# Kernel optimization log

Hardware: AMD Instinct MI355X
Metric: run time of the kernel (lower is better)

## Reference

```python
import jax, jax.numpy as jnp
import numpy as np

PATCH = 3
COMPLETENESS = 2.0


def setup_inputs() -> dict:
    key = jax.random.key(0)
    k1, k2, k3 = jax.random.split(key, 3)
    C, Hs, Ws, Hr, Wr = 64, 512, 512, 512, 512
    ref = jax.random.normal(k1, (C, Hr, Wr), dtype=jnp.float32)
    nnf_sr = jax.random.randint(k2, (Hs, Ws, 2), 0, 512, dtype=jnp.int32)  # (ry, rx) per src pixel
    nnf_rs = jax.random.randint(k3, (Hr, Wr, 2), 0, 512, dtype=jnp.int32)  # (sy, sx) per ref pixel
    return {"ref": ref, "nnf_sr": nnf_sr, "nnf_rs": nnf_rs}


def bds_vote(ref, nnf_sr, nnf_rs, patch=PATCH, completeness=COMPLETENESS):
    C, Hr, Wr = ref.shape
    Hs, Ws = nnf_sr.shape[0], nnf_sr.shape[1]
    h = patch // 2
    ws = 1.0 / (Hs * Ws)
    wr = completeness / (Hr * Wr)

    guide = jnp.zeros((C, Hs * Ws), dtype=ref.dtype)
    weight = jnp.zeros((Hs * Ws,), dtype=ref.dtype)

    def accumulate(guide, weight, sy, sx, ry, rx, w):
        # sy,sx: target (src) centers [N]; ry,rx: source (ref) centers [N]
        # Clipped patch extents of the original code are equivalent to per-pixel
        # validity: both target and ref offset coords must be in range.
        for dy in range(-h, h + 1):
            for dx in range(-h, h + 1):
                ty, tx = sy + dy, sx + dx
                qy, qx = ry + dy, rx + dx
                valid = ((ty >= 0) & (ty < Hs) & (tx >= 0) & (tx < Ws) &
                         (qy >= 0) & (qy < Hr) & (qx >= 0) & (qx < Wr))
                vmask = valid.astype(ref.dtype) * w
                idx = jnp.clip(ty, 0, Hs - 1) * Ws + jnp.clip(tx, 0, Ws - 1)
                vals = ref[:, jnp.clip(qy, 0, Hr - 1), jnp.clip(qx, 0, Wr - 1)] * vmask[None, :]
                guide = guide.at[:, idx].add(vals)
                weight = weight.at[idx].add(vmask)
        return guide, weight

    # source -> reference pass (weight ws)
    gy, gx = jnp.meshgrid(jnp.arange(Hs), jnp.arange(Ws), indexing='ij')
    guide, weight = accumulate(guide, weight,
                               gy.reshape(-1), gx.reshape(-1),
                               nnf_sr[..., 0].reshape(-1), nnf_sr[..., 1].reshape(-1), ws)
    # reference -> source pass (weight wr)
    ry, rx = jnp.meshgrid(jnp.arange(Hr), jnp.arange(Wr), indexing='ij')
    guide, weight = accumulate(guide, weight,
                               nnf_rs[..., 0].reshape(-1), nnf_rs[..., 1].reshape(-1),
                               ry.reshape(-1), rx.reshape(-1), wr)

    weight = jnp.where(weight == 0, jnp.asarray(1.0, ref.dtype), weight)
    return (guide / weight[None, :]).reshape(C, Hs, Ws)


def reference(ref, nnf_sr, nnf_rs):
    return bds_vote(ref, nnf_sr, nnf_rs)
```

## Files before the change

### kernel.cpp

```cpp
#include <hip/hip_runtime.h>

#define HS   512
#define WSZ  512
#define NC   64
#define HW   (HS * WSZ)
#define KCAP 16
#define LCAP 32

typedef unsigned int uint;
typedef unsigned short ushort;

__device__ __forceinline__ ushort f2bf(float f) {
    uint b = __float_as_uint(f);
    return (ushort)((b + 0x7FFFu + ((b >> 16) & 1u)) >> 16);
}

__global__ __launch_bounds__(256) void prep_kernel(
    const float4* __restrict__ ref4, uint4* __restrict__ refu4,
    int* __restrict__ cnt)
{
    __shared__ float lds[64 * 65];
    const int p0  = blockIdx.x * 64;
    const int tid = threadIdx.x;
    if (tid < 64) cnt[blockIdx.x * 64 + tid] = 0;
#pragma unroll
    for (int k = 0; k < 4; ++k) {
        int e  = k * 256 + tid;
        int c  = e >> 4;
        int i4 = e & 15;
        float4 v = ref4[(size_t)c * (HW / 4) + (p0 >> 2) + i4];
        lds[(i4 * 4 + 0) * 65 + c] = v.x;
        lds[(i4 * 4 + 1) * 65 + c] = v.y;
        lds[(i4 * 4 + 2) * 65 + c] = v.z;
        lds[(i4 * 4 + 3) * 65 + c] = v.w;
    }
    __syncthreads();
#pragma unroll
    for (int k = 0; k < 2; ++k) {
        int e = k * 256 + tid;
        int i = e >> 3;
        int q = e & 7;
        const float* row = &lds[i * 65 + 8 * q];
        uint4 u;
        u.x = (uint)f2bf(row[0]) | ((uint)f2bf(row[1]) << 16);
        u.y = (uint)f2bf(row[2]) | ((uint)f2bf(row[3]) << 16);
        u.z = (uint)f2bf(row[4]) | ((uint)f2bf(row[5]) << 16);
        u.w = (uint)f2bf(row[6]) | ((uint)f2bf(row[7]) << 16);
        refu4[(size_t)(p0 + i) * 8 + q] = u;
    }
}

__global__ __launch_bounds__(256) void fill_bins(
    const int2* __restrict__ nnf_rs, int* __restrict__ cnt,
    int* __restrict__ slots)
{
    int r = blockIdx.x * 256 + threadIdx.x;
    int2 s = nnf_rs[r];
    int bin = (s.x << 9) | s.y;
    int pos = atomicAdd(&cnt[bin], 1);
    if (pos < KCAP) slots[(bin << 4) + pos] = r;
}

__global__ __launch_bounds__(256) void gather_lds(
    const uint4* __restrict__ refu4,
    const int2*  __restrict__ nnf_sr,
    const int*   __restrict__ cnt,
    const int*   __restrict__ slots,
    float* __restrict__ out)
{
    const float ws = 1.0f / 262144.0f;
    const float wr = 2.0f / 262144.0f;

    __shared__ int lists[32][36];
    __shared__ int lcnt[32];
    __shared__ int bcnt[102];

    const int tid = threadIdx.x;
    const int t0  = blockIdx.x * 32;
    const int ty0 = t0 >> 9, tx0 = t0 & 511;

    if (tid < 32) lcnt[tid] = 0;
    if (tid < 102) {
        const int jr = tid / 34, jc = tid - jr * 34;
        const int sy = ty0 + jr - 1, sx = tx0 + jc - 1;
        const bool sv = ((unsigned)sy < 512u) & ((unsigned)sx < 512u);
        bcnt[tid] = sv ? min(cnt[(sy << 9) | sx], KCAP) : 0;
    }
    __syncthreads();

    for (int p = tid; p < 306; p += 256) {
        const int j  = p / 3;
        const int di = p - j * 3;
        const int jr = j / 34, jc = j - jr * 34;
        const int dy = 1 - jr;
        const int dx = di - 1;
        const int lt = jc - 1 + dx;
        const int c  = bcnt[j];
        if (((unsigned)lt < 32u) && (c > 0)) {
            const int sy = ty0 + jr - 1, sx = tx0 + jc - 1;
            const int sbase = (((sy << 9) | sx) << 4);
            for (int e = 0; e < c; ++e) {
                const int r  = slots[sbase + e];
                const int qy = (r >> 9) + dy, qx = (r & 511) + dx;
                if (((unsigned)qy < 512u) & ((unsigned)qx < 512u)) {
                    const int pos = atomicAdd(&lcnt[lt], 1);
                    if (pos < LCAP) lists[lt][pos] = (qy << 9) | qx;
                }
            }
        }
    }
    __syncthreads();

    const int k  = tid & 7;
    const int lt = tid >> 3;
    const int t  = t0 + lt;
    const int ty = ty0, tx = t & 511;

    float a0=0,a1=0,a2=0,a3=0,a4=0,a5=0,a6=0,a7=0, w=0.f;

#define ACCUM(qv, mv)                                                         \
    {                                                                         \
        const int   q_ = (qv);                                                \
        const float m_ = (mv);                                                \
        uint4 u_ = refu4[(size_t)q_ * 8 + k];                                 \
        a0 += __uint_as_float(u_.x << 16)         * m_;                       \
        a1 += __uint_as_float(u_.x & 0xffff0000u) * m_;                       \
        a2 += __uint_as_float(u_.y << 16)         * m_;                       \
        a3 += __uint_as_float(u_.y & 0xffff0000u) * m_;                       \
        a4 += __uint_as_float(u_.z << 16)         * m_;                       \
        a5 += __uint_as_float(u_.z & 0xffff0000u) * m_;                       \
        a6 += __uint_as_float(u_.w << 16)         * m_;                       \
        a7 += __uint_as_float(u_.w & 0xffff0000u) * m_;                       \
        w += m_;                                                              \
    }

#define TAP(dy, dx)                                                           \
    {                                                                         \
        const int sy = ty - (dy), sx = tx - (dx);                             \
        const bool sval = ((unsigned)sy < 512u) & ((unsigned)sx < 512u);      \
        const int sidx = ((sy & 511) << 9) | (sx & 511);                      \
        const int2 nn = nnf_sr[sidx];                                         \
        const int qy = nn.x + (dy), qx = nn.y + (dx);                         \
        const bool v = sval & ((unsigned)qy < 512u) & ((unsigned)qx < 512u);  \
        ACCUM((((qy & 511) << 9) | (qx & 511)), v ? ws : 0.f)                 \
    }

    TAP(-1, -1)  TAP(-1, 0)  TAP(-1, 1)
    TAP( 0, -1)  TAP( 0, 0)  TAP( 0, 1)
    TAP( 1, -1)  TAP( 1, 0)  TAP( 1, 1)
#undef TAP

    const int S = min(lcnt[lt], LCAP);
    for (int s = 0; s < S; s += 4) {
        const int4 e4 = *(const int4*)&lists[lt][s];
        ACCUM(e4.x & 0x3FFFF, wr)
        ACCUM(e4.y & 0x3FFFF, (s + 1 < S) ? wr : 0.f)
        ACCUM(e4.z & 0x3FFFF, (s + 2 < S) ? wr : 0.f)
        ACCUM(e4.w & 0x3FFFF, (s + 3 < S) ? wr : 0.f)
    }
#undef ACCUM

    if (w == 0.f) w = 1.f;
    const float inv = 1.f / w;
    size_t o = (size_t)(8 * k) * HW + t;
    out[o]                = a0 * inv;
    out[o + 1*(size_t)HW] = a1 * inv;
    out[o + 2*(size_t)HW] = a2 * inv;
    out[o + 3*(size_t)HW] = a3 * inv;
    out[o + 4*(size_t)HW] = a4 * inv;
    out[o + 5*(size_t)HW] = a5 * inv;
    out[o + 6*(size_t)HW] = a6 * inv;
    out[o + 7*(size_t)HW] = a7 * inv;
}

__global__ __launch_bounds__(256) void gather8_f32(
    const float* __restrict__ reff,
    const int2*  __restrict__ nnf_sr,
    const int*   __restrict__ cnt,
    const int*   __restrict__ slots,
    float* __restrict__ out)
{
    const float ws = 1.0f / 262144.0f;
    const float wr = 2.0f / 262144.0f;

    const int tid = threadIdx.x;
    const int k   = tid & 7;
    const int t   = blockIdx.x * 32 + (tid >> 3);
    const int ty  = t >> 9, tx = t & 511;

    float a0=0,a1=0,a2=0,a3=0,a4=0,a5=0,a6=0,a7=0, w=0.f;

#define ACCUM(qv, mv)                                                         \
    {                                                                         \
        const int   q_ = (qv);                                                \
        const float m_ = (mv);                                                \
        const size_t c0_ = (size_t)(8 * k) * HW + q_;                         \
        a0 += reff[c0_ + 0*(size_t)HW] * m_;                                  \
        a1 += reff[c0_ + 1*(size_t)HW] * m_;                                  \
        a2 += reff[c0_ + 2*(size_t)HW] * m_;                                  \
        a3 += reff[c0_ + 3*(size_t)HW] * m_;                                  \
        a4 += reff[c0_ + 4*(size_t)HW] * m_;                                  \
        a5 += reff[c0_ + 5*(size_t)HW] * m_;                                  \
        a6 += reff[c0_ + 6*(size_t)HW] * m_;                                  \
        a7 += reff[c0_ + 7*(size_t)HW] * m_;                                  \
        w += m_;                                                              \
    }

    int mt0,mt1,mt2,mt3,mt4,mt5,mt6,mt7,mt8;
    int run = 0;

#define TAP(i, dy, dx)                                                        \
    {                                                                         \
        const int sy = ty - (dy), sx = tx - (dx);                             \
        const bool sval = ((unsigned)sy < 512u) & ((unsigned)sx < 512u);      \
        const int sidx = ((sy & 511) << 9) | (sx & 511);                      \
        mt##i = (sidx << 12) | ((i) << 8) | run;                              \
        const int c = cnt[sidx];                                              \
        run += sval ? min(c, KCAP) : 0;                                       \
        const int2 nn = nnf_sr[sidx];                                         \
        const int qy = nn.x + (dy), qx = nn.y + (dx);                         \
        const bool v = sval & ((unsigned)qy < 512u) & ((unsigned)qx < 512u);  \
        ACCUM((((qy & 511) << 9) | (qx & 511)), v ? ws : 0.f)                 \
    }

    TAP(0, -1, -1)  TAP(1, -1, 0)  TAP(2, -1, 1)
    TAP(3,  0, -1)  TAP(4,  0, 0)  TAP(5,  0, 1)
    TAP(6,  1, -1)  TAP(7,  1, 0)  TAP(8,  1, 1)
#undef TAP

    const int S = run;

#define SEL(i)  m_ = (s_ >= (mt##i & 255)) ? mt##i : m_;
#define ENTRY(sv)                                                             \
    {                                                                         \
        const int s_ = (sv);                                                  \
        int m_ = mt0;                                                         \
        SEL(1) SEL(2) SEL(3) SEL(4) SEL(5) SEL(6) SEL(7) SEL(8)               \
        const int off_ = m_ & 255;                                            \
        const int ii_  = (m_ >> 8) & 15;                                      \
        const int bs_  = (m_ >> 12) << 4;                                     \
        const int idx_ = min(s_ - off_, KCAP - 1);                            \
        const int e_   = slots[bs_ + idx_];                                   \
        const int ry_  = (e_ >> 9) & 511, rx_ = e_ & 511;                     \
        const int dyp_ = (ii_ * 11) >> 5;                                     \
        const int dy_  = dyp_ - 1, dx_ = ii_ - 3 * dyp_ - 1;                  \
        const int qy_  = ry_ + dy_, qx_ = rx_ + dx_;                          \
        const bool v_  = (s_ < S) &                                           \
                         ((unsigned)qy_ < 512u) & ((unsigned)qx_ < 512u);     \
        ACCUM((((qy_ & 511) << 9) | (qx_ & 511)), v_ ? wr : 0.f)              \
    }

    for (int s = 0; s < S; s += 2) {
        ENTRY(s)
        ENTRY(s + 1)
    }
#undef ENTRY
#undef SEL
#undef ACCUM

    if (w == 0.f) w = 1.f;
    const float inv = 1.f / w;
    size_t o = (size_t)(8 * k) * HW + t;
    out[o]                = a0 * inv;
    out[o + 1*(size_t)HW] = a1 * inv;
    out[o + 2*(size_t)HW] = a2 * inv;
    out[o + 3*(size_t)HW] = a3 * inv;
    out[o + 4*(size_t)HW] = a4 * inv;
    out[o + 5*(size_t)HW] = a5 * inv;
    out[o + 6*(size_t)HW] = a6 * inv;
    out[o + 7*(size_t)HW] = a7 * inv;
}

extern "C" void kernel_launch(void* const* d_in, const int* in_sizes, int n_in,
                              void* d_out, int out_size, void* d_ws, size_t ws_size,
                              hipStream_t stream)
{
    const float* ref    = (const float*)d_in[0];
    const int2*  nnf_sr = (const int2*)d_in[1];
    const int2*  nnf_rs = (const int2*)d_in[2];
    float* out = (float*)d_out;

    char* wsb = (char*)d_ws;
    const size_t refT_bytes = (size_t)HW * NC * 2;
    const size_t cnt_bytes  = (size_t)HW * 4;
    const size_t slot_bytes = (size_t)HW * KCAP * 4;

    if (ws_size >= refT_bytes + cnt_bytes + slot_bytes) {
        uint4* refu4 = (uint4*)wsb;
        int*   cntp  = (int*)(wsb + refT_bytes);
        int*   slots = (int*)(wsb + refT_bytes + cnt_bytes);

        prep_kernel<<<HW / 64, 256, 0, stream>>>((const float4*)ref, refu4, cntp);
        fill_bins<<<HW / 256, 256, 0, stream>>>(nnf_rs, cntp, slots);
        gather_lds<<<HW / 32, 256, 0, stream>>>(refu4, nnf_sr, cntp, slots, out);
    } else {
        int* cntp  = (int*)wsb;
        int* slots = cntp + HW;
        hipMemsetAsync(cntp, 0, cnt_bytes, stream);
        fill_bins<<<HW / 256, 256, 0, stream>>>(nnf_rs, cntp, slots);
        gather8_f32<<<HW / 32, 256, 0, stream>>>(ref, nnf_sr, cntp, slots, out);
    }
}
```

Baseline: 227.4 us.

## Merge prep and bin fill into one launch; sentinel-padded unweighted accumulation

Merges the bf16 transpose kernel and the nnf_rs binning kernel into one launch, with blocks split by index, and zeroes the counts with a memset instead. In the gather kernel, the block's 102 source NNF entries are staged in LDS. Invalid taps and list padding now read a zero sentinel row instead of multiplying by a weight mask, so accumulation becomes plain adds. The ws/wr weights are applied once at the end from valid-entry counts. The costs are one extra memset launch and a workspace row of zeros, and the single final scale may round slightly differently from the per-tap weighting.

Result: faster. 217.5 us (-4.3%).

```diff
diff --git a/kernel.cpp b/kernel.cpp
--- a/kernel.cpp
+++ b/kernel.cpp
@@ -6,6 +6,7 @@
 #define HW   (HS * WSZ)
 #define KCAP 16
 #define LCAP 32
+#define SENT 0x40000
 
 typedef unsigned int uint;
 typedef unsigned short ushort;
@@ -15,50 +16,52 @@
     return (ushort)((b + 0x7FFFu + ((b >> 16) & 1u)) >> 16);
 }
 
-__global__ __launch_bounds__(256) void prep_kernel(
+__global__ __launch_bounds__(256) void prep_fill(
     const float4* __restrict__ ref4, uint4* __restrict__ refu4,
-    int* __restrict__ cnt)
-{
-    __shared__ float lds[64 * 65];
-    const int p0  = blockIdx.x * 64;
-    const int tid = threadIdx.x;
-    if (tid < 64) cnt[blockIdx.x * 64 + tid] = 0;
-#pragma unroll
-    for (int k = 0; k < 4; ++k) {
-        int e  = k * 256 + tid;
-        int c  = e >> 4;
-        int i4 = e & 15;
-        float4 v = ref4[(size_t)c * (HW / 4) + (p0 >> 2) + i4];
-        lds[(i4 * 4 + 0) * 65 + c] = v.x;
-        lds[(i4 * 4 + 1) * 65 + c] = v.y;
-        lds[(i4 * 4 + 2) * 65 + c] = v.z;
-        lds[(i4 * 4 + 3) * 65 + c] = v.w;
-    }
-    __syncthreads();
-#pragma unroll
-    for (int k = 0; k < 2; ++k) {
-        int e = k * 256 + tid;
-        int i = e >> 3;
-        int q = e & 7;
-        const float* row = &lds[i * 65 + 8 * q];
-        uint4 u;
-        u.x = (uint)f2bf(row[0]) | ((uint)f2bf(row[1]) << 16);
-        u.y = (uint)f2bf(row[2]) | ((uint)f2bf(row[3]) << 16);
-        u.z = (uint)f2bf(row[4]) | ((uint)f2bf(row[5]) << 16);
-        u.w = (uint)f2bf(row[6]) | ((uint)f2bf(row[7]) << 16);
-        refu4[(size_t)(p0 + i) * 8 + q] = u;
-    }
-}
-
-__global__ __launch_bounds__(256) void fill_bins(
     const int2* __restrict__ nnf_rs, int* __restrict__ cnt,
     int* __restrict__ slots)
 {
-    int r = blockIdx.x * 256 + threadIdx.x;
-    int2 s = nnf_rs[r];
-    int bin = (s.x << 9) | s.y;
-    int pos = atomicAdd(&cnt[bin], 1);
-    if (pos < KCAP) slots[(bin << 4) + pos] = r;
+    __shared__ float lds[64 * 65];
+    const int tid = threadIdx.x;
+
+    if (blockIdx.x < 4096) {
+        const int p0 = blockIdx.x * 64;
+#pragma unroll
+        for (int k = 0; k < 4; ++k) {
+            int e  = k * 256 + tid;
+            int c  = e >> 4;
+            int i4 = e & 15;
+            float4 v = ref4[(size_t)c * (HW / 4) + (p0 >> 2) + i4];
+            lds[(i4 * 4 + 0) * 65 + c] = v.x;
+            lds[(i4 * 4 + 1) * 65 + c] = v.y;
+            lds[(i4 * 4 + 2) * 65 + c] = v.z;
+            lds[(i4 * 4 + 3) * 65 + c] = v.w;
+        }
+        __syncthreads();
+#pragma unroll
+        for (int k = 0; k < 2; ++k) {
+            int e = k * 256 + tid;
+            int i = e >> 3;
+            int q = e & 7;
+            const float* row = &lds[i * 65 + 8 * q];
+            uint4 u;
+            u.x = (uint)f2bf(row[0]) | ((uint)f2bf(row[1]) << 16);
+            u.y = (uint)f2bf(row[2]) | ((uint)f2bf(row[3]) << 16);
+            u.z = (uint)f2bf(row[4]) | ((uint)f2bf(row[5]) << 16);
+            u.w = (uint)f2bf(row[6]) | ((uint)f2bf(row[7]) << 16);
+            refu4[(size_t)(p0 + i) * 8 + q] = u;
+        }
+    } else {
+        if (blockIdx.x == 4096 && tid < 8) {
+            uint4 z; z.x = 0u; z.y = 0u; z.z = 0u; z.w = 0u;
+            refu4[(size_t)HW * 8 + tid] = z;
+        }
+        const int r = (blockIdx.x - 4096) * 256 + tid;
+        const int2 s = nnf_rs[r];
+        const int bin = (s.x << 9) | s.y;
+        const int pos = atomicAdd(&cnt[bin], 1);
+        if (pos < KCAP) slots[(bin << 4) + pos] = r;
+    }
 }
 
 __global__ __launch_bounds__(256) void gather_lds(
@@ -71,9 +74,10 @@
     const float ws = 1.0f / 262144.0f;
     const float wr = 2.0f / 262144.0f;
 
-    __shared__ int lists[32][36];
-    __shared__ int lcnt[32];
-    __shared__ int bcnt[102];
+    __shared__ __align__(16) int lists[32][36];
+    __shared__ int  lcnt[32];
+    __shared__ int  bcnt[102];
+    __shared__ int2 snn[102];
 
     const int tid = threadIdx.x;
     const int t0  = blockIdx.x * 32;
@@ -84,7 +88,14 @@
         const int jr = tid / 34, jc = tid - jr * 34;
         const int sy = ty0 + jr - 1, sx = tx0 + jc - 1;
         const bool sv = ((unsigned)sy < 512u) & ((unsigned)sx < 512u);
-        bcnt[tid] = sv ? min(cnt[(sy << 9) | sx], KCAP) : 0;
+        const int sidx = ((sy & 511) << 9) | (sx & 511);
+        bcnt[tid] = sv ? min(cnt[sidx], KCAP) : 0;
+        snn[tid]  = nnf_sr[sidx];
+    }
+    {
+        int4 s4; s4.x = SENT; s4.y = SENT; s4.z = SENT; s4.w = SENT;
+        for (int p = tid; p < 288; p += 256)
+            ((int4*)lists)[p] = s4;
     }
     __syncthreads();
 
@@ -113,36 +124,34 @@
 
     const int k  = tid & 7;
     const int lt = tid >> 3;
-    const int t  = t0 + lt;
-    const int ty = ty0, tx = t & 511;
-
-    float a0=0,a1=0,a2=0,a3=0,a4=0,a5=0,a6=0,a7=0, w=0.f;
-
-#define ACCUM(qv, mv)                                                         \
-    {                                                                         \
-        const int   q_ = (qv);                                                \
-        const float m_ = (mv);                                                \
-        uint4 u_ = refu4[(size_t)q_ * 8 + k];                                 \
-        a0 += __uint_as_float(u_.x << 16)         * m_;                       \
-        a1 += __uint_as_float(u_.x & 0xffff0000u) * m_;                       \
-        a2 += __uint_as_float(u_.y << 16)         * m_;                       \
-        a3 += __uint_as_float(u_.y & 0xffff0000u) * m_;                       \
-        a4 += __uint_as_float(u_.z << 16)         * m_;                       \
-        a5 += __uint_as_float(u_.z & 0xffff0000u) * m_;                       \
-        a6 += __uint_as_float(u_.w << 16)         * m_;                       \
-        a7 += __uint_as_float(u_.w & 0xffff0000u) * m_;                       \
-        w += m_;                                                              \
+
+    float a0=0,a1=0,a2=0,a3=0,a4=0,a5=0,a6=0,a7=0;
+    int nv = 0;
+
+#define ACCUM(qv)                                                             \
+    {                                                                         \
+        const uint4 u_ = refu4[(size_t)(qv) * 8 + k];                         \
+        a0 += __uint_as_float(u_.x << 16);                                    \
+        a1 += __uint_as_float(u_.x & 0xffff0000u);                            \
+        a2 += __uint_as_float(u_.y << 16);                                    \
+        a3 += __uint_as_float(u_.y & 0xffff0000u);                            \
+        a4 += __uint_as_float(u_.z << 16);                                    \
+        a5 += __uint_as_float(u_.z & 0xffff0000u);                            \
+        a6 += __uint_as_float(u_.w << 16);                                    \
+        a7 += __uint_as_float(u_.w & 0xffff0000u);                            \
     }
 
 #define TAP(dy, dx)                                                           \
     {                                                                         \
-        const int sy = ty - (dy), sx = tx - (dx);                             \
-        const bool sval = ((unsigned)sy < 512u) & ((unsigned)sx < 512u);      \
-        const int sidx = ((sy & 511) << 9) | (sx & 511);                      \
-        const int2 nn = nnf_sr[sidx];                                         \
+        const bool rv = ((unsigned)(ty0 - (dy)) < 512u);         \
+        const bool cv = ((unsigned)(tx0 + lt - (dx)) < 512u);                 \
+        const int2 nn = snn[(1 - (dy)) * 34 + (lt - (dx) + 1)];               \
         const int qy = nn.x + (dy), qx = nn.y + (dx);                         \
-        const bool v = sval & ((unsigned)qy < 512u) & ((unsigned)qx < 512u);  \
-        ACCUM((((qy & 511) << 9) | (qx & 511)), v ? ws : 0.f)                 \
+        const bool v = rv & cv &                                              \
+                       ((unsigned)qy < 512u) & ((unsigned)qx < 512u);         \
+        const int q = v ? ((qy << 9) | qx) : SENT;                            \
+        nv += v ? 1 : 0;                                                      \
+        ACCUM(q)                                                              \
     }
 
     TAP(-1, -1)  TAP(-1, 0)  TAP(-1, 1)
@@ -150,27 +159,43 @@
     TAP( 1, -1)  TAP( 1, 0)  TAP( 1, 1)
 #undef TAP
 
-    const int S = min(lcnt[lt], LCAP);
-    for (int s = 0; s < S; s += 4) {
+    a0 *= 0.5f; a1 *= 0.5f; a2 *= 0.5f; a3 *= 0.5f;
+    a4 *= 0.5f; a5 *= 0.5f; a6 *= 0.5f; a7 *= 0.5f;
+
+    const int Sreal = min(lcnt[lt], LCAP);
+    const int S4 = (Sreal + 3) & ~3;
+    for (int s = 0; s < S4; s += 4) {
         const int4 e4 = *(const int4*)&lists[lt][s];
-        ACCUM(e4.x & 0x3FFFF, wr)
-        ACCUM(e4.y & 0x3FFFF, (s + 1 < S) ? wr : 0.f)
-        ACCUM(e4.z & 0x3FFFF, (s + 2 < S) ? wr : 0.f)
-        ACCUM(e4.w & 0x3FFFF, (s + 3 < S) ? wr : 0.f)
+        ACCUM(e4.x)
+        ACCUM(e4.y)
+        ACCUM(e4.z)
+        ACCUM(e4.w)
     }
 #undef ACCUM
 
-    if (w == 0.f) w = 1.f;
-    const float inv = 1.f / w;
+    const float wsum = ws * (float)nv + wr * (float)Sreal;
+    const float sc = wr / wsum;
+    const int t = t0 + lt;
     size_t o = (size_t)(8 * k) * HW + t;
-    out[o]                = a0 * inv;
-    out[o + 1*(size_t)HW] = a1 * inv;
-    out[o + 2*(size_t)HW] = a2 * inv;
-    out[o + 3*(size_t)HW] = a3 * inv;
-    out[o + 4*(size_t)HW] = a4 * inv;
-    out[o + 5*(size_t)HW] = a5 * inv;
-    out[o + 6*(size_t)HW] = a6 * inv;
-    out[o + 7*(size_t)HW] = a7 * inv;
+    out[o]                = a0 * sc;
+    out[o + 1*(size_t)HW] = a1 * sc;
+    out[o + 2*(size_t)HW] = a2 * sc;
+    out[o + 3*(size_t)HW] = a3 * sc;
+    out[o + 4*(size_t)HW] = a4 * sc;
+    out[o + 5*(size_t)HW] = a5 * sc;
+    out[o + 6*(size_t)HW] = a6 * sc;
+    out[o + 7*(size_t)HW] = a7 * sc;
+}
+
+__global__ __launch_bounds__(256) void fill_bins(
+    const int2* __restrict__ nnf_rs, int* __restrict__ cnt,
+    int* __restrict__ slots)
+{
+    int r = blockIdx.x * 256 + threadIdx.x;
+    int2 s = nnf_rs[r];
+    int bin = (s.x << 9) | s.y;
+    int pos = atomicAdd(&cnt[bin], 1);
+    if (pos < KCAP) slots[(bin << 4) + pos] = r;
 }
 
 __global__ __launch_bounds__(256) void gather8_f32(
@@ -216,7 +241,7 @@
         const int sidx = ((sy & 511) << 9) | (sx & 511);                      \
         mt##i = (sidx << 12) | ((i) << 8) | run;                              \
         const int c = cnt[sidx];                                              \
-        run += sval ? min(c, KCAP) : 0;                                       \
+        run += sval ? min(c, KCAP) : 0;                                      \
         const int2 nn = nnf_sr[sidx];                                         \
         const int qy = nn.x + (dy), qx = nn.y + (dx);                         \
         const bool v = sval & ((unsigned)qy < 512u) & ((unsigned)qx < 512u);  \
@@ -281,7 +306,7 @@
     float* out = (float*)d_out;
 
     char* wsb = (char*)d_ws;
-    const size_t refT_bytes = (size_t)HW * NC * 2;
+    const size_t refT_bytes = (size_t)HW * NC * 2 + 128;
     const size_t cnt_bytes  = (size_t)HW * 4;
     const size_t slot_bytes = (size_t)HW * KCAP * 4;
 
@@ -290,8 +315,9 @@
         int*   cntp  = (int*)(wsb + refT_bytes);
         int*   slots = (int*)(wsb + refT_bytes + cnt_bytes);
 
-        prep_kernel<<<HW / 64, 256, 0, stream>>>((const float4*)ref, refu4, cntp);
-        fill_bins<<<HW / 256, 256, 0, stream>>>(nnf_rs, cntp, slots);
+        hipMemsetAsync(cntp, 0, cnt_bytes, stream);
+        prep_fill<<<4096 + HW / 256, 256, 0, stream>>>(
+            (const float4*)ref, refu4, nnf_rs, cntp, slots);
         gather_lds<<<HW / 32, 256, 0, stream>>>(refu4, nnf_sr, cntp, slots, out);
     } else {
         int* cntp  = (int*)wsb;
```
